# Optimization experiments

Hardware: AMD Instinct MI355X
Metric: run time of the kernel (lower is better)

## Reference

```python
import jax, jax.numpy as jnp
import numpy as np

B, S, D, H, FF, P = 16, 200, 512, 8, 2048, 10
HD = D // H
EPS = 1e-5


def _pe2d(h, w, ch):
    # Faithful numpy port of PositionalEncoding2D (positional_encodings lib)
    channels = int(np.ceil(ch / 4) * 2)
    inv_freq = 1.0 / (10000.0 ** (np.arange(0, channels, 2, dtype=np.float32) / channels))
    sin_x = np.einsum('i,j->ij', np.arange(h, dtype=np.float32), inv_freq)
    sin_y = np.einsum('i,j->ij', np.arange(w, dtype=np.float32), inv_freq)
    emb_x = np.stack([np.sin(sin_x), np.cos(sin_x)], -1).reshape(h, channels)
    emb_y = np.stack([np.sin(sin_y), np.cos(sin_y)], -1).reshape(w, channels)
    emb = np.zeros((h, w, 2 * channels), dtype=np.float32)
    emb[:, :, :channels] = emb_x[:, None, :]
    emb[:, :, channels:2 * channels] = emb_y[None, :, :]
    return emb[:, :, :ch]


def _xavier(key, shape):
    fan_out, fan_in = shape
    lim = float(np.sqrt(6.0 / (fan_in + fan_out)))
    return jax.random.uniform(key, shape, minval=-lim, maxval=lim, dtype=jnp.float32)


def setup_inputs():
    key = jax.random.key(0)
    ks = jax.random.split(key, 8)
    x = jax.random.normal(ks[0], (B, S, D), dtype=jnp.float32)
    pos = jnp.asarray(_pe2d(S, S, P))  # (S, S, P) positional bias features
    Wkv = _xavier(ks[1], (2 * D, D)); bkv = jnp.zeros((2 * D,))
    Wo = _xavier(ks[2], (D, D)); bo = jnp.zeros((D,))
    Wpos = _xavier(ks[3], (1, P)); bpos = jnp.zeros((1,))
    W1 = _xavier(ks[4], (FF, D)); b1 = jnp.zeros((FF,))
    W2 = _xavier(ks[5], (D, FF)); b2 = jnp.zeros((D,))
    g1 = jnp.ones((D,)); beta1 = jnp.zeros((D,))
    g2 = jnp.ones((D,)); beta2 = jnp.zeros((D,))
    return {"x": x, "pos": pos, "Wkv": Wkv, "bkv": bkv, "Wo": Wo, "bo": bo,
            "Wpos": Wpos, "bpos": bpos, "W1": W1, "b1": b1, "W2": W2, "b2": b2,
            "g1": g1, "beta1": beta1, "g2": g2, "beta2": beta2}


def _layernorm(x, g, b):
    mu = jnp.mean(x, axis=-1, keepdims=True)
    var = jnp.mean(jnp.square(x - mu), axis=-1, keepdims=True)
    return (x - mu) * jax.lax.rsqrt(var + EPS) * g + b


def reference(x, pos, Wkv, bkv, Wo, bo, Wpos, bpos, W1, b1, W2, b2, g1, beta1, g2, beta2):
    # --- MultiheadAttention_KV (attn_type='kv') ---
    kv = x @ Wkv.T + bkv                                   # (B,S,2D)
    kv = kv.reshape(B, S, H, 2 * HD).transpose(0, 2, 1, 3)  # (B,H,S,2hd)
    k, v = kv[..., :HD], kv[..., HD:]
    attn = jnp.einsum('bhid,bhjd->bhij', k, k) / jnp.sqrt(jnp.float32(HD))
    # map_pos is linear: map_pos(attn[...,None] + pos) == attn*sum(w) + (pos@w + b)
    # -> same math as materializing the (B,H,S,S,P) tensor, but fused.
    pos_bias = pos @ Wpos[0] + bpos[0]                     # (S,S)
    scores = attn * jnp.sum(Wpos) + pos_bias[None, None]
    a = jax.nn.softmax(scores, axis=-1)
    vals = jnp.einsum('bhij,bhjd->bhid', a, v)             # (B,H,S,hd)
    vals = vals.transpose(0, 2, 1, 3).reshape(B, S, D)
    o = vals @ Wo.T + bo
    # --- residual + post-norm ---
    h = _layernorm(x + o, g1, beta1)
    # --- FFN ---
    ff = jax.nn.relu(h @ W1.T + b1) @ W2.T + b2
    return _layernorm(h + ff, g2, beta2)
```

## Files before the change

kernel.cpp:

```cpp
#include <hip/hip_runtime.h>
#include <hip/hip_bf16.h>

#define EPSV 1e-5f
static const int B_ = 16, S_ = 200, D_ = 512, H_ = 8, FF_ = 2048, P_ = 10, HD_ = 64;
static const int SP = 224;

typedef __bf16 bf16_t;
typedef __attribute__((ext_vector_type(8))) __bf16 bf16x8;
typedef __attribute__((ext_vector_type(4))) __bf16 bf16x4;
typedef __attribute__((ext_vector_type(4))) float f32x4;

__device__ __forceinline__ void gload16(const void* g, void* l) {
    __builtin_amdgcn_global_load_lds(
        (const __attribute__((address_space(1))) void*)g,
        (__attribute__((address_space(3))) void*)l, 16, 0, 0);
}

template <int BM, int BN, int WROWS, int WCOLS, int EPI>
__global__ __launch_bounds__(256) void mfma_gemm(
    const bf16_t* __restrict__ A,
    const bf16_t* __restrict__ Bw,
    float* __restrict__ Cf, bf16_t* __restrict__ Cb, long cBat, int ldc,
    const float* __restrict__ bias,
    bf16_t* __restrict__ kOut, bf16_t* __restrict__ vtOut,
    int M, int N, int K, int kcPerSplit)
{
    constexpr int MR = WROWS / 16, NR = WCOLS / 16;
    constexpr int NWC = BN / WCOLS;
    static_assert((4 / NWC) * WROWS == BM, "wave tiling must cover BM");
    static_assert(NWC * WCOLS == BN, "wave tiling must cover BN");

    __shared__ bf16_t Asm[BM * 64];
    __shared__ bf16_t Bsm[BN * 64];

    const int wv = threadIdx.x >> 6;
    const int ln = threadIdx.x & 63;
    const int split = blockIdx.z;
    const int rowBase = blockIdx.y * BM;
    const int colBase = blockIdx.x * BN;
    const int wr = (wv / NWC) * WROWS;
    const int wc = (wv % NWC) * WCOLS;

    const int lr8 = ln >> 3;
    const int lc = (ln & 7) * 8;

    f32x4 acc[MR][NR] = {};

    const int kBeg = split * kcPerSplit;
    const int kEnd = kBeg + kcPerSplit;

    for (int k0 = kBeg; k0 < kEnd; k0 += 64) {
        #pragma unroll
        for (int i = 0; i < BM / 32; i++) {
            int row = i * 32 + wv * 8 + lr8;
            int gr = rowBase + row; gr = (gr < M) ? gr : (M - 1);
            gload16(A + (long)gr * K + k0 + lc, &Asm[(i * 32 + wv * 8) * 64]);
        }
        #pragma unroll
        for (int i = 0; i < BN / 32; i++) {
            int col = i * 32 + wv * 8 + lr8;
            int gc = colBase + col; gc = (gc < N) ? gc : (N - 1);
            gload16(Bw + (long)gc * K + k0 + lc, &Bsm[(i * 32 + wv * 8) * 64]);
        }
        __syncthreads();

        #pragma unroll
        for (int kk = 0; kk < 2; kk++) {
            bf16x8 af[MR], bfr[NR];
            #pragma unroll
            for (int m = 0; m < MR; m++)
                af[m] = *reinterpret_cast<const bf16x8*>(
                    &Asm[(wr + m * 16 + (ln & 15)) * 64 + kk * 32 + (ln >> 4) * 8]);
            #pragma unroll
            for (int n = 0; n < NR; n++)
                bfr[n] = *reinterpret_cast<const bf16x8*>(
                    &Bsm[(wc + n * 16 + (ln & 15)) * 64 + kk * 32 + (ln >> 4) * 8]);
            #pragma unroll
            for (int m = 0; m < MR; m++)
                #pragma unroll
                for (int n = 0; n < NR; n++)
                    acc[m][n] = __builtin_amdgcn_mfma_f32_16x16x32_bf16(
                        af[m], bfr[n], acc[m][n], 0, 0, 0);
        }
        __syncthreads();
    }

    #pragma unroll
    for (int m = 0; m < MR; m++) {
        #pragma unroll
        for (int n = 0; n < NR; n++) {
            #pragma unroll
            for (int r = 0; r < 4; r++) {
                int row = rowBase + wr + m * 16 + (ln >> 4) * 4 + r;
                int col = colBase + wc + n * 16 + (ln & 15);
                if (row >= M || col >= N) continue;
                float v = acc[m][n][r];
                if constexpr (EPI == 3) {
                    v += bias[col];
                    int b = row / S_, s = row - b * S_;
                    int h = col >> 7, w = col & 127;
                    if (w < HD_)
                        kOut[((long)(b * H_ + h) * SP + s) * HD_ + w] = (bf16_t)v;
                    else
                        vtOut[((long)(b * H_ + h) * HD_ + (w - HD_)) * SP + s] = (bf16_t)v;
                } else if constexpr (EPI == 1) {
                    v += bias[col];
                    v = fmaxf(v, 0.f);
                    Cb[(long)row * ldc + col] = (bf16_t)v;
                } else {
                    Cf[(long)split * cBat + (long)row * ldc + col] = v;
                }
            }
        }
    }
}

__global__ __launch_bounds__(256) void attn_fused(
    const bf16_t* __restrict__ Kb, const bf16_t* __restrict__ Vt,
    const float* __restrict__ G, const float* __restrict__ scalePtr,
    bf16_t* __restrict__ vals)
{
    __shared__ __align__(16) bf16_t Pl[4][16][232];

    const int bh = blockIdx.x;
    const int tile = blockIdx.y;
    const int wv = threadIdx.x >> 6;
    const int ln = threadIdx.x & 63;
    const int b = bh >> 3, h = bh & 7;
    const int rowBase = tile * 64 + wv * 16;

    const bf16_t* Kbh = Kb + (long)bh * SP * HD_;
    const bf16_t* Vbh = Vt + (long)bh * HD_ * SP;
    const float scale = scalePtr[0];

    const int lr = ln & 15;
    const int lk = (ln >> 4) * 8;

    f32x4 acc[14];
    #pragma unroll
    for (int n = 0; n < 14; n++) acc[n] = (f32x4){0.f, 0.f, 0.f, 0.f};

    int arow = rowBase + lr; arow = (arow < S_) ? arow : (S_ - 1);
    const bf16x8 a0 = *reinterpret_cast<const bf16x8*>(Kbh + (long)arow * HD_ + lk);
    const bf16x8 a1 = *reinterpret_cast<const bf16x8*>(Kbh + (long)arow * HD_ + 32 + lk);

    #pragma unroll
    for (int n = 0; n < 14; n++) {
        const bf16_t* bp = Kbh + (long)(n * 16 + lr) * HD_;
        bf16x8 b0 = *reinterpret_cast<const bf16x8*>(bp + lk);
        bf16x8 b1 = *reinterpret_cast<const bf16x8*>(bp + 32 + lk);
        acc[n] = __builtin_amdgcn_mfma_f32_16x16x32_bf16(a0, b0, acc[n], 0, 0, 0);
        acc[n] = __builtin_amdgcn_mfma_f32_16x16x32_bf16(a1, b1, acc[n], 0, 0, 0);
    }

    float Gc[14];
    #pragma unroll
    for (int n = 0; n < 14; n++) Gc[n] = G[n * 16 + lr];

    #pragma unroll
    for (int r = 0; r < 4; r++) {
        float m = -1e30f;
        #pragma unroll
        for (int n = 0; n < 14; n++) {
            float v = acc[n][r] * scale + Gc[n];
            acc[n][r] = v;
            m = fmaxf(m, v);
        }
        #pragma unroll
        for (int off = 1; off < 16; off <<= 1) m = fmaxf(m, __shfl_xor(m, off));
        float s = 0.f;
        #pragma unroll
        for (int n = 0; n < 14; n++) {
            float e = __expf(acc[n][r] - m);
            acc[n][r] = e;
            s += e;
        }
        #pragma unroll
        for (int off = 1; off < 16; off <<= 1) s += __shfl_xor(s, off);
        float inv = 1.f / s;
        #pragma unroll
        for (int n = 0; n < 14; n++) acc[n][r] *= inv;
    }

    #pragma unroll
    for (int n = 0; n < 14; n++)
        #pragma unroll
        for (int r = 0; r < 4; r++)
            Pl[wv][(ln >> 4) * 4 + r][n * 16 + lr] = (bf16_t)acc[n][r];

    f32x4 vacc[4] = {};
    #pragma unroll
    for (int kk = 0; kk < 7; kk++) {
        bf16x8 pa = *reinterpret_cast<const bf16x8*>(&Pl[wv][lr][kk * 32 + lk]);
        #pragma unroll
        for (int n = 0; n < 4; n++) {
            bf16x8 vb = *reinterpret_cast<const bf16x8*>(
                Vbh + (long)(n * 16 + lr) * SP + kk * 32 + lk);
            vacc[n] = __builtin_amdgcn_mfma_f32_16x16x32_bf16(pa, vb, vacc[n], 0, 0, 0);
        }
    }

    #pragma unroll
    for (int n = 0; n < 4; n++) {
        #pragma unroll
        for (int r = 0; r < 4; r++) {
            int row = rowBase + (ln >> 4) * 4 + r;
            if (row < S_)
                vals[((long)b * S_ + row) * D_ + h * HD_ + n * 16 + lr] =
                    (bf16_t)vacc[n][r];
        }
    }
}

__global__ __launch_bounds__(256) void prep_all(
    const float* __restrict__ x, const float* __restrict__ Wkv,
    const float* __restrict__ Wo, const float* __restrict__ W1,
    const float* __restrict__ W2, bf16_t* __restrict__ dst,
    float4* __restrict__ zeroP,
    const float* __restrict__ pos, const float* __restrict__ Wpos,
    float* __restrict__ G, float* __restrict__ scal)
{
    const int gid = blockIdx.x * blockDim.x + threadIdx.x;
    const int nthr = gridDim.x * blockDim.x;

    for (int i = gid; i < 1130496; i += nthr) {
        long e = (long)i * 4;
        const float* s; long off;
        if (e < 1638400)      { s = x;   off = e; }
        else if (e < 2162688) { s = Wkv; off = e - 1638400; }
        else if (e < 2424832) { s = Wo;  off = e - 2162688; }
        else if (e < 3473408) { s = W1;  off = e - 2424832; }
        else                  { s = W2;  off = e - 3473408; }
        float4 v = *reinterpret_cast<const float4*>(s + off);
        bf16x4 o = {(bf16_t)v.x, (bf16_t)v.y, (bf16_t)v.z, (bf16_t)v.w};
        *reinterpret_cast<bf16x4*>(dst + e) = o;
    }
    for (int i = gid; i < 458752; i += nthr)
        zeroP[i] = make_float4(0.f, 0.f, 0.f, 0.f);
    if (gid < SP) {
        float g = -1e30f;
        if (gid < S_) {
            g = 0.f;
            #pragma unroll
            for (int p = 6; p < 10; p++) g += pos[(long)gid * P_ + p] * Wpos[p];
        }
        G[gid] = g;
    }
    if (gid == 0) {
        float sw = 0.f;
        for (int p = 0; p < P_; p++) sw += Wpos[p];
        scal[0] = sw * 0.125f;
    }
}

template <int NPART>
__global__ __launch_bounds__(256) void add_ln_p(
    const float* __restrict__ a, const float* __restrict__ parts, long partStride,
    const float* __restrict__ bias,
    const float* __restrict__ g, const float* __restrict__ beta,
    float* __restrict__ outf, bf16_t* __restrict__ outb, int rows)
{
    int row = blockIdx.x * 4 + (threadIdx.x >> 6);
    int lane = threadIdx.x & 63;
    if (row >= rows) return;
    long base = (long)row * D_;
    float v[8];
    float sum = 0.f;
    #pragma unroll
    for (int i = 0; i < 8; i++) {
        int c = lane + i * 64;
        float t = a[base + c] + bias[c];
        #pragma unroll
        for (int p = 0; p < NPART; p++) t += parts[p * partStride + base + c];
        v[i] = t;
        sum += t;
    }
    #pragma unroll
    for (int off = 32; off; off >>= 1) sum += __shfl_xor(sum, off);
    float mean = sum * (1.f / 512.f);
    float var = 0.f;
    #pragma unroll
    for (int i = 0; i < 8; i++) { float d = v[i] - mean; var += d * d; }
    #pragma unroll
    for (int off = 32; off; off >>= 1) var += __shfl_xor(var, off);
    float rstd = rsqrtf(var * (1.f / 512.f) + EPSV);
    #pragma unroll
    for (int i = 0; i < 8; i++) {
        int c = lane + i * 64;
        float o = (v[i] - mean) * rstd * g[c] + beta[c];
        outf[base + c] = o;
        if (outb) outb[base + c] = (bf16_t)o;
    }
}

extern "C" void kernel_launch(void* const* d_in, const int* in_sizes, int n_in,
                              void* d_out, int out_size, void* d_ws, size_t ws_size,
                              hipStream_t stream)
{
    const float* x    = (const float*)d_in[0];
    const float* pos  = (const float*)d_in[1];
    const float* Wkv  = (const float*)d_in[2];
    const float* bkv  = (const float*)d_in[3];
    const float* Wo   = (const float*)d_in[4];
    const float* bo   = (const float*)d_in[5];
    const float* Wpos = (const float*)d_in[6];
    const float* W1   = (const float*)d_in[8];
    const float* b1   = (const float*)d_in[9];
    const float* W2   = (const float*)d_in[10];
    const float* b2   = (const float*)d_in[11];
    const float* g1   = (const float*)d_in[12];
    const float* be1  = (const float*)d_in[13];
    const float* g2   = (const float*)d_in[14];
    const float* be2  = (const float*)d_in[15];
    float* out = (float*)d_out;

    char* w = (char*)d_ws;
    bf16_t* xb   = (bf16_t*)(w + 0);
    bf16_t* Wkvb = (bf16_t*)(w + 3276800);
    bf16_t* Wob  = (bf16_t*)(w + 4325376);
    bf16_t* W1b  = (bf16_t*)(w + 4849664);
    bf16_t* W2b  = (bf16_t*)(w + 6946816);
    bf16_t* Kb   = (bf16_t*)(w + 9043968);
    bf16_t* Vt   = (bf16_t*)(w + 12713984);
    float*  G    = (float*)(w + 16384000);
    float*  scal = (float*)(w + 16384896);
    bf16_t* vals = (bf16_t*)(w + 16385024);
    float*  hf   = (float*)(w + 19661824);
    bf16_t* hb   = (bf16_t*)(w + 26215424);
    float*  obuf = (float*)(w + 29492224);
    bf16_t* tb   = (bf16_t*)(w + 42599424);
    float*  fbuf = (float*)(w + 55706624);

    const int M = B_ * S_;
    const long PS = (long)M * D_;

    prep_all<<<2048, 256, 0, stream>>>(x, Wkv, Wo, W1, W2, xb, (float4*)Kb,
                                       pos, Wpos, G, scal);

    mfma_gemm<128, 64, 64, 32, 3><<<dim3(16, 25, 1), 256, 0, stream>>>(
        xb, Wkvb, nullptr, nullptr, 0, 0, bkv, Kb, Vt, M, 2 * D_, D_, D_);

    attn_fused<<<dim3(128, 4, 1), 256, 0, stream>>>(Kb, Vt, G, scal, vals);

    mfma_gemm<128, 64, 64, 32, 5><<<dim3(8, 25, 2), 256, 0, stream>>>(
        vals, Wob, obuf, nullptr, PS, D_, nullptr, nullptr, nullptr, M, D_, D_, 256);

    add_ln_p<2><<<(M + 3) / 4, 256, 0, stream>>>(x, obuf, PS, bo, g1, be1, hf, hb, M);

    mfma_gemm<128, 64, 64, 32, 1><<<dim3(32, 25, 1), 256, 0, stream>>>(
        hb, W1b, nullptr, tb, 0, FF_, b1, nullptr, nullptr, M, FF_, D_, D_);

    mfma_gemm<128, 64, 64, 32, 5><<<dim3(8, 25, 2), 256, 0, stream>>>(
        tb, W2b, fbuf, nullptr, PS, D_, nullptr, nullptr, nullptr, M, D_, FF_, 1024);

    add_ln_p<2><<<(M + 3) / 4, 256, 0, stream>>>(hf, fbuf, PS, b2, g2, be2, out, nullptr, M);
}
```

Baseline: 115.0 us.

## Double-buffer GEMM LDS tiles with async prefetch and XOR-swizzled layout

```diff
diff --git a/kernel.cpp b/kernel.cpp
--- a/kernel.cpp
+++ b/kernel.cpp
@@ -27,11 +27,13 @@
 {
     constexpr int MR = WROWS / 16, NR = WCOLS / 16;
     constexpr int NWC = BN / WCOLS;
+    constexpr int NLOADS = BM / 32 + BN / 32;
     static_assert((4 / NWC) * WROWS == BM, "wave tiling must cover BM");
     static_assert(NWC * WCOLS == BN, "wave tiling must cover BN");
-
-    __shared__ bf16_t Asm[BM * 64];
-    __shared__ bf16_t Bsm[BN * 64];
+    static_assert(NLOADS == 6, "vmcnt literal below assumes 6 loads/stage");
+
+    __shared__ bf16_t Asm[2][BM * 64];
+    __shared__ bf16_t Bsm[2][BN * 64];
 
     const int wv = threadIdx.x >> 6;
     const int ln = threadIdx.x & 63;
@@ -42,39 +44,44 @@
     const int wc = (wv % NWC) * WCOLS;
 
     const int lr8 = ln >> 3;
-    const int lc = (ln & 7) * 8;
+    const int csw = ((ln & 7) ^ lr8) * 8;
 
     f32x4 acc[MR][NR] = {};
 
     const int kBeg = split * kcPerSplit;
     const int kEnd = kBeg + kcPerSplit;
 
-    for (int k0 = kBeg; k0 < kEnd; k0 += 64) {
+    auto STAGE = [&](int k0, int buf) {
         #pragma unroll
         for (int i = 0; i < BM / 32; i++) {
             int row = i * 32 + wv * 8 + lr8;
             int gr = rowBase + row; gr = (gr < M) ? gr : (M - 1);
-            gload16(A + (long)gr * K + k0 + lc, &Asm[(i * 32 + wv * 8) * 64]);
+            gload16(A + (long)gr * K + k0 + csw, &Asm[buf][(i * 32 + wv * 8) * 64]);
         }
         #pragma unroll
         for (int i = 0; i < BN / 32; i++) {
             int col = i * 32 + wv * 8 + lr8;
             int gc = colBase + col; gc = (gc < N) ? gc : (N - 1);
-            gload16(Bw + (long)gc * K + k0 + lc, &Bsm[(i * 32 + wv * 8) * 64]);
-        }
-        __syncthreads();
-
+            gload16(Bw + (long)gc * K + k0 + csw, &Bsm[buf][(i * 32 + wv * 8) * 64]);
+        }
+    };
+
+    auto COMPUTE = [&](int buf) {
         #pragma unroll
         for (int kk = 0; kk < 2; kk++) {
             bf16x8 af[MR], bfr[NR];
             #pragma unroll
-            for (int m = 0; m < MR; m++)
-                af[m] = *reinterpret_cast<const bf16x8*>(
-                    &Asm[(wr + m * 16 + (ln & 15)) * 64 + kk * 32 + (ln >> 4) * 8]);
-            #pragma unroll
-            for (int n = 0; n < NR; n++)
-                bfr[n] = *reinterpret_cast<const bf16x8*>(
-                    &Bsm[(wc + n * 16 + (ln & 15)) * 64 + kk * 32 + (ln >> 4) * 8]);
+            for (int m = 0; m < MR; m++) {
+                int r = wr + m * 16 + (ln & 15);
+                int pc = (kk * 4 + (ln >> 4)) ^ (r & 7);
+                af[m] = *reinterpret_cast<const bf16x8*>(&Asm[buf][r * 64 + pc * 8]);
+            }
+            #pragma unroll
+            for (int n = 0; n < NR; n++) {
+                int r = wc + n * 16 + (ln & 15);
+                int pc = (kk * 4 + (ln >> 4)) ^ (r & 7);
+                bfr[n] = *reinterpret_cast<const bf16x8*>(&Bsm[buf][r * 64 + pc * 8]);
+            }
             #pragma unroll
             for (int m = 0; m < MR; m++)
                 #pragma unroll
@@ -82,7 +89,26 @@
                     acc[m][n] = __builtin_amdgcn_mfma_f32_16x16x32_bf16(
                         af[m], bfr[n], acc[m][n], 0, 0, 0);
         }
-        __syncthreads();
+    };
+
+    STAGE(kBeg, 0);
+
+    int t = 0;
+    for (int k0 = kBeg; k0 < kEnd; k0 += 64, ++t) {
+        const bool has_next = (k0 + 64 < kEnd);
+        if (has_next) {
+            STAGE(k0 + 64, (t + 1) & 1);
+            asm volatile("s_waitcnt vmcnt(6)" ::: "memory");
+        } else {
+            asm volatile("s_waitcnt vmcnt(0)" ::: "memory");
+        }
+        __builtin_amdgcn_s_barrier();
+        __builtin_amdgcn_sched_barrier(0);
+        COMPUTE(t & 1);
+        if (has_next) {
+            __builtin_amdgcn_sched_barrier(0);
+            __builtin_amdgcn_s_barrier();
+        }
     }
 
     #pragma unroll
```

Result: no change. 116.6 us (+1.3%).
